# Performance work log

Hardware: AMD Instinct MI355X
Metric: run time of the kernel (lower is better)

The kernel has to match this reference:

```python
import jax, jax.numpy as jnp
import numpy as np
import itertools

LUT_DIM = 33  # 33x33x33 color LUT, as in Generator3DLUT_zero(dim=33)


def setup_inputs() -> dict:
    key = jax.random.key(0)
    k1, k2 = jax.random.split(key)
    # RGB image batch in [0,1]: [B, 3, H, W]
    x = jax.random.uniform(k1, (4, 3, 1080, 1920), dtype=jnp.float32)
    # Learned LUT parameter: [3, dim, dim, dim] (channels, b-axis, g-axis, r-axis)
    LUT = jax.random.normal(k2, (3, LUT_DIM, LUT_DIM, LUT_DIM), dtype=jnp.float32)
    return {"x": x, "LUT": LUT}


def _trilinear_lut(x, LUT, dim):
    # x: [B,3,H,W] in [0,1]; LUT: [3,dim,dim,dim] indexed [channel, b, g, r]
    # (r varies fastest, matching the original CUDA trilinear_forward kernel
    #  where flat index = r + g*dim + b*dim*dim).
    scaled = jnp.clip(x, 0.0, 1.0) * (dim - 1)          # [B,3,H,W]
    idx = jnp.clip(jnp.floor(scaled).astype(jnp.int32), 0, dim - 2)
    frac = scaled - idx.astype(scaled.dtype)            # in [0,1]
    r_id, g_id, b_id = idx[:, 0], idx[:, 1], idx[:, 2]   # each [B,H,W]
    fr, fg, fb = frac[:, 0], frac[:, 1], frac[:, 2]      # each [B,H,W]

    out = jnp.zeros_like(x)  # [B,3,H,W]
    for dr, dg, db in itertools.product((0, 1), repeat=3):  # 8 corners
        w = (jnp.where(dr, fr, 1.0 - fr)
             * jnp.where(dg, fg, 1.0 - fg)
             * jnp.where(db, fb, 1.0 - fb))               # [B,H,W]
        corner = LUT[:, b_id + db, g_id + dg, r_id + dr]  # [3,B,H,W] gather
        out = out + w[:, None] * jnp.transpose(corner, (1, 0, 2, 3))
    return out


def reference(x, LUT):
    return _trilinear_lut(x, LUT, LUT_DIM)
```

## Files before the change

kernel.cpp:

```cpp
#include <hip/hip_runtime.h>
#include <hip/hip_fp16.h>

#define DIM  33
#define DIM2 1089
#define DIM3 35937
#define HW   2073600
#define NPIX 8294400

typedef float  vf4 __attribute__((ext_vector_type(4)));
typedef _Float16 vh8 __attribute__((ext_vector_type(8)));

union F4H {
    vf4      f4;
    _Float16 h[8];
};

__global__ __launch_bounds__(256) void pack_lut8_kernel(
        const float* __restrict__ lut, vf4* __restrict__ lut8) {
    int i = blockIdx.x * blockDim.x + threadIdx.x;
    if (i >= DIM3) return;
    int b   = i / DIM2;
    int rem = i - b * DIM2;
    int g   = rem / DIM;
    int r   = rem - g * DIM;
    int b1 = min(b + 1, DIM - 1);
    int g1 = min(g + 1, DIM - 1);
    int r1 = min(r + 1, DIM - 1);

    _Float16 h[32];
#pragma unroll
    for (int db = 0; db < 2; ++db)
#pragma unroll
        for (int dg = 0; dg < 2; ++dg)
#pragma unroll
            for (int dr = 0; dr < 2; ++dr) {
                int bb = db ? b1 : b;
                int gg = dg ? g1 : g;
                int rr = dr ? r1 : r;
                int base = bb * DIM2 + gg * DIM + rr;
                int ci = ((db * 2 + dg) * 2 + dr) * 3;
                h[ci + 0] = (_Float16)lut[base];
                h[ci + 1] = (_Float16)lut[base + DIM3];
                h[ci + 2] = (_Float16)lut[base + 2 * DIM3];
            }
#pragma unroll
    for (int k = 24; k < 32; ++k) h[k] = (_Float16)0.0f;

    const vf4* hv = (const vf4*)h;
    vf4* dst = lut8 + (size_t)i * 4;
    dst[0] = hv[0];
    dst[1] = hv[1];
    dst[2] = hv[2];
    dst[3] = hv[3];
}

__device__ __forceinline__ void trilerp8(
        float r, float g, float b, const vf4* __restrict__ lut8,
        float& o0, float& o1, float& o2) {
    float rs = fminf(fmaxf(r, 0.0f), 1.0f) * 32.0f;
    float gs = fminf(fmaxf(g, 0.0f), 1.0f) * 32.0f;
    float bs = fminf(fmaxf(b, 0.0f), 1.0f) * 32.0f;
    int ri = min((int)rs, 31);
    int gi = min((int)gs, 31);
    int bi = min((int)bs, 31);
    float fr = rs - (float)ri;
    float fg = gs - (float)gi;
    float fb = bs - (float)bi;

    const vf4* e = lut8 + (size_t)(bi * DIM2 + gi * DIM + ri) * 4;
    F4H q0, q1, q2;
    q0.f4 = e[0];
    q1.f4 = e[1];
    q2.f4 = e[2];

    float c[24];
#pragma unroll
    for (int j = 0; j < 8; ++j) {
        c[j]      = (float)q0.h[j];
        c[8 + j]  = (float)q1.h[j];
        c[16 + j] = (float)q2.h[j];
    }

    float wr[2] = {1.0f - fr, fr};
    float wg[2] = {1.0f - fg, fg};
    float wb[2] = {1.0f - fb, fb};
    float a0 = 0.0f, a1 = 0.0f, a2 = 0.0f;
#pragma unroll
    for (int db = 0; db < 2; ++db)
#pragma unroll
        for (int dg = 0; dg < 2; ++dg) {
            float wbg = wb[db] * wg[dg];
#pragma unroll
            for (int dr = 0; dr < 2; ++dr) {
                float w = wbg * wr[dr];
                int ci = ((db * 2 + dg) * 2 + dr) * 3;
                a0 = fmaf(w, c[ci + 0], a0);
                a1 = fmaf(w, c[ci + 1], a1);
                a2 = fmaf(w, c[ci + 2], a2);
            }
        }
    o0 = a0; o1 = a1; o2 = a2;
}

__global__ __launch_bounds__(256) void lut_apply_fp16x8(
        const float* __restrict__ x, const vf4* __restrict__ lut8,
        float* __restrict__ out) {
    int i4 = blockIdx.x * blockDim.x + threadIdx.x;
    const int HW4 = HW / 4;
    if (i4 >= NPIX / 4) return;
    int n   = i4 / HW4;
    int rem = i4 - n * HW4;
    size_t base = (size_t)n * (size_t)(3 * HW) + (size_t)rem * 4;

    const vf4 rv = __builtin_nontemporal_load((const vf4*)(x + base));
    const vf4 gv = __builtin_nontemporal_load((const vf4*)(x + base + HW));
    const vf4 bv = __builtin_nontemporal_load((const vf4*)(x + base + 2 * (size_t)HW));

    float oa[4], ob[4], oc[4];
#pragma unroll
    for (int k = 0; k < 4; ++k) {
        trilerp8(rv[k], gv[k], bv[k], lut8, oa[k], ob[k], oc[k]);
    }
    vf4 o0 = {oa[0], oa[1], oa[2], oa[3]};
    vf4 o1 = {ob[0], ob[1], ob[2], ob[3]};
    vf4 o2 = {oc[0], oc[1], oc[2], oc[3]};
    __builtin_nontemporal_store(o0, (vf4*)(out + base));
    __builtin_nontemporal_store(o1, (vf4*)(out + base + HW));
    __builtin_nontemporal_store(o2, (vf4*)(out + base + 2 * (size_t)HW));
}

extern "C" void kernel_launch(void* const* d_in, const int* in_sizes, int n_in,
                              void* d_out, int out_size, void* d_ws, size_t ws_size,
                              hipStream_t stream) {
    const float* x   = (const float*)d_in[0];
    const float* lut = (const float*)d_in[1];
    float* out = (float*)d_out;

    const int groups = NPIX / 4;
    const int blocks = (groups + 255) / 256;

    vf4* lut8 = (vf4*)d_ws;
    pack_lut8_kernel<<<(DIM3 + 255) / 256, 256, 0, stream>>>(lut, lut8);
    lut_apply_fp16x8<<<blocks, 256, 0, stream>>>(x, lut8, out);
}
```

Before: 225.8 us.

## Quantize LUT to packed 8-bit and gather from LDS in persistent kernel

Finds the LUT's max absolute value, then packs it as one 32-bit word per node holding three unsigned 8-bit channels. The whole 144KB table is loaded into LDS by a persistent 1024-thread block per CU, and chunks of pixels are pulled from an atomic work counter. Each pixel's eight corner reads now come from LDS instead of scattered global/L2 gathers, and results are dequantized with a single scale and bias. The trade-off is a much coarser LUT (8-bit versus fp16), a risk of LDS bank conflicts, and extra small pre-kernels plus a memset.

```diff
diff --git a/kernel.cpp b/kernel.cpp
--- a/kernel.cpp
+++ b/kernel.cpp
@@ -1,19 +1,157 @@
 #include <hip/hip_runtime.h>
-#include <hip/hip_fp16.h>
 
 #define DIM  33
 #define DIM2 1089
 #define DIM3 35937
 #define HW   2073600
+#define HW4  518400
 #define NPIX 8294400
-
-typedef float  vf4 __attribute__((ext_vector_type(4)));
-typedef _Float16 vh8 __attribute__((ext_vector_type(8)));
-
-union F4H {
-    vf4      f4;
-    _Float16 h[8];
-};
+#define GROUPS (NPIX / 4)
+#define CHUNK  4096
+#define NCHUNK ((GROUPS + CHUNK - 1) / CHUNK)
+#define LDS_BYTES (DIM3 * 4)
+#define MAIN_BLOCKS  256
+#define MAIN_THREADS 1024
+
+typedef float vf4 __attribute__((ext_vector_type(4)));
+
+#define TBL_OFF 64
+
+__device__ __forceinline__ float ub(unsigned v, int b) {
+    return (float)((v >> (8 * b)) & 0xffu);
+}
+
+__global__ __launch_bounds__(256) void lut_maxabs_kernel(
+        const float* __restrict__ lut, unsigned* __restrict__ maxbits) {
+    int i = blockIdx.x * 256 + threadIdx.x;
+    float m = 0.0f;
+    if (i < 3 * DIM3) m = fabsf(lut[i]);
+#pragma unroll
+    for (int off = 32; off > 0; off >>= 1)
+        m = fmaxf(m, __shfl_down(m, off, 64));
+    if ((threadIdx.x & 63) == 0)
+        atomicMax(maxbits, __float_as_uint(m));
+}
+
+__global__ __launch_bounds__(256) void pack_lut_u8_kernel(
+        const float* __restrict__ lut, const unsigned* __restrict__ maxbits,
+        unsigned* __restrict__ tbl) {
+    int i = blockIdx.x * 256 + threadIdx.x;
+    if (i >= DIM3) return;
+    float mx  = fmaxf(__uint_as_float(*maxbits), 1e-20f);
+    float inv = 127.0f / mx;
+    int q0 = min(max(__float2int_rn(lut[i]            * inv) + 128, 0), 255);
+    int q1 = min(max(__float2int_rn(lut[i + DIM3]     * inv) + 128, 0), 255);
+    int q2 = min(max(__float2int_rn(lut[i + 2 * DIM3] * inv) + 128, 0), 255);
+    tbl[i] = (unsigned)q0 | ((unsigned)q1 << 8) | ((unsigned)q2 << 16);
+}
+
+extern __shared__ unsigned s_tbl[];
+
+__global__ __launch_bounds__(MAIN_THREADS, 1) void lut_apply_lds(
+        const float* __restrict__ x, const unsigned* __restrict__ tbl,
+        unsigned* __restrict__ ctr, const unsigned* __restrict__ maxbits,
+        float* __restrict__ out) {
+    __shared__ unsigned chunk_s;
+    for (int i = threadIdx.x; i < DIM3; i += MAIN_THREADS)
+        s_tbl[i] = tbl[i];
+    __syncthreads();
+
+    const float mx   = fmaxf(__uint_as_float(*maxbits), 1e-20f);
+    const float s_   = mx * (1.0f / 127.0f);
+    const float bias = -128.0f * s_;
+
+    for (;;) {
+        if (threadIdx.x == 0) chunk_s = atomicAdd(ctr, 1u);
+        __syncthreads();
+        unsigned c = chunk_s;
+        __syncthreads();
+        if (c >= NCHUNK) return;
+
+        int gend = min((int)((c + 1) * CHUNK), GROUPS);
+        for (int g = (int)(c * CHUNK) + threadIdx.x; g < gend; g += MAIN_THREADS) {
+            int n   = g / HW4;
+            int rem = g - n * HW4;
+            size_t base = (size_t)n * (size_t)(3 * HW) + (size_t)rem * 4;
+
+            const vf4 rv = __builtin_nontemporal_load((const vf4*)(x + base));
+            const vf4 gv = __builtin_nontemporal_load((const vf4*)(x + base + HW));
+            const vf4 bv = __builtin_nontemporal_load((const vf4*)(x + base + 2 * (size_t)HW));
+
+            float oa[4], ob[4], oc[4];
+#pragma unroll
+            for (int k = 0; k < 4; ++k) {
+                float rs = fminf(fmaxf(rv[k], 0.0f), 1.0f) * 32.0f;
+                float gs = fminf(fmaxf(gv[k], 0.0f), 1.0f) * 32.0f;
+                float bs = fminf(fmaxf(bv[k], 0.0f), 1.0f) * 32.0f;
+                int ri = min((int)rs, 31);
+                int gi = min((int)gs, 31);
+                int bi = min((int)bs, 31);
+                float fr = rs - (float)ri;
+                float fg = gs - (float)gi;
+                float fb = bs - (float)bi;
+
+                int i00 = bi * DIM2 + gi * DIM + ri;
+                unsigned c000 = s_tbl[i00];
+                unsigned c001 = s_tbl[i00 + 1];
+                unsigned c010 = s_tbl[i00 + DIM];
+                unsigned c011 = s_tbl[i00 + DIM + 1];
+                unsigned c100 = s_tbl[i00 + DIM2];
+                unsigned c101 = s_tbl[i00 + DIM2 + 1];
+                unsigned c110 = s_tbl[i00 + DIM2 + DIM];
+                unsigned c111 = s_tbl[i00 + DIM2 + DIM + 1];
+
+                float wr1 = fr, wr0 = 1.0f - fr;
+                float wg1 = fg, wg0 = 1.0f - fg;
+                float wb1 = fb, wb0 = 1.0f - fb;
+                float wb0g0 = wb0 * wg0, wb0g1 = wb0 * wg1;
+                float wb1g0 = wb1 * wg0, wb1g1 = wb1 * wg1;
+                float w000 = wb0g0 * wr0, w001 = wb0g0 * wr1;
+                float w010 = wb0g1 * wr0, w011 = wb0g1 * wr1;
+                float w100 = wb1g0 * wr0, w101 = wb1g0 * wr1;
+                float w110 = wb1g1 * wr0, w111 = wb1g1 * wr1;
+
+                float a0, a1, a2;
+                a0 =      w000 * ub(c000, 0);
+                a1 =      w000 * ub(c000, 1);
+                a2 =      w000 * ub(c000, 2);
+                a0 = fmaf(w001,  ub(c001, 0), a0);
+                a1 = fmaf(w001,  ub(c001, 1), a1);
+                a2 = fmaf(w001,  ub(c001, 2), a2);
+                a0 = fmaf(w010,  ub(c010, 0), a0);
+                a1 = fmaf(w010,  ub(c010, 1), a1);
+                a2 = fmaf(w010,  ub(c010, 2), a2);
+                a0 = fmaf(w011,  ub(c011, 0), a0);
+                a1 = fmaf(w011,  ub(c011, 1), a1);
+                a2 = fmaf(w011,  ub(c011, 2), a2);
+                a0 = fmaf(w100,  ub(c100, 0), a0);
+                a1 = fmaf(w100,  ub(c100, 1), a1);
+                a2 = fmaf(w100,  ub(c100, 2), a2);
+                a0 = fmaf(w101,  ub(c101, 0), a0);
+                a1 = fmaf(w101,  ub(c101, 1), a1);
+                a2 = fmaf(w101,  ub(c101, 2), a2);
+                a0 = fmaf(w110,  ub(c110, 0), a0);
+                a1 = fmaf(w110,  ub(c110, 1), a1);
+                a2 = fmaf(w110,  ub(c110, 2), a2);
+                a0 = fmaf(w111,  ub(c111, 0), a0);
+                a1 = fmaf(w111,  ub(c111, 1), a1);
+                a2 = fmaf(w111,  ub(c111, 2), a2);
+
+                oa[k] = fmaf(s_, a0, bias);
+                ob[k] = fmaf(s_, a1, bias);
+                oc[k] = fmaf(s_, a2, bias);
+            }
+            vf4 s0 = {oa[0], oa[1], oa[2], oa[3]};
+            vf4 s1 = {ob[0], ob[1], ob[2], ob[3]};
+            vf4 s2 = {oc[0], oc[1], oc[2], oc[3]};
+            __builtin_nontemporal_store(s0, (vf4*)(out + base));
+            __builtin_nontemporal_store(s1, (vf4*)(out + base + HW));
+            __builtin_nontemporal_store(s2, (vf4*)(out + base + 2 * (size_t)HW));
+        }
+    }
+}
+
+union F4H { vf4 f4; _Float16 h[8]; };
 
 __global__ __launch_bounds__(256) void pack_lut8_kernel(
         const float* __restrict__ lut, vf4* __restrict__ lut8) {
@@ -26,7 +164,6 @@
     int b1 = min(b + 1, DIM - 1);
     int g1 = min(g + 1, DIM - 1);
     int r1 = min(r + 1, DIM - 1);
-
     _Float16 h[32];
 #pragma unroll
     for (int db = 0; db < 2; ++db)
@@ -45,88 +182,68 @@
             }
 #pragma unroll
     for (int k = 24; k < 32; ++k) h[k] = (_Float16)0.0f;
-
     const vf4* hv = (const vf4*)h;
     vf4* dst = lut8 + (size_t)i * 4;
-    dst[0] = hv[0];
-    dst[1] = hv[1];
-    dst[2] = hv[2];
-    dst[3] = hv[3];
-}
-
-__device__ __forceinline__ void trilerp8(
-        float r, float g, float b, const vf4* __restrict__ lut8,
-        float& o0, float& o1, float& o2) {
-    float rs = fminf(fmaxf(r, 0.0f), 1.0f) * 32.0f;
-    float gs = fminf(fmaxf(g, 0.0f), 1.0f) * 32.0f;
-    float bs = fminf(fmaxf(b, 0.0f), 1.0f) * 32.0f;
-    int ri = min((int)rs, 31);
-    int gi = min((int)gs, 31);
-    int bi = min((int)bs, 31);
-    float fr = rs - (float)ri;
-    float fg = gs - (float)gi;
-    float fb = bs - (float)bi;
-
-    const vf4* e = lut8 + (size_t)(bi * DIM2 + gi * DIM + ri) * 4;
-    F4H q0, q1, q2;
-    q0.f4 = e[0];
-    q1.f4 = e[1];
-    q2.f4 = e[2];
-
-    float c[24];
-#pragma unroll
-    for (int j = 0; j < 8; ++j) {
-        c[j]      = (float)q0.h[j];
-        c[8 + j]  = (float)q1.h[j];
-        c[16 + j] = (float)q2.h[j];
-    }
-
-    float wr[2] = {1.0f - fr, fr};
-    float wg[2] = {1.0f - fg, fg};
-    float wb[2] = {1.0f - fb, fb};
-    float a0 = 0.0f, a1 = 0.0f, a2 = 0.0f;
-#pragma unroll
-    for (int db = 0; db < 2; ++db)
-#pragma unroll
-        for (int dg = 0; dg < 2; ++dg) {
-            float wbg = wb[db] * wg[dg];
-#pragma unroll
-            for (int dr = 0; dr < 2; ++dr) {
-                float w = wbg * wr[dr];
-                int ci = ((db * 2 + dg) * 2 + dr) * 3;
-                a0 = fmaf(w, c[ci + 0], a0);
-                a1 = fmaf(w, c[ci + 1], a1);
-                a2 = fmaf(w, c[ci + 2], a2);
-            }
-        }
-    o0 = a0; o1 = a1; o2 = a2;
+    dst[0] = hv[0]; dst[1] = hv[1]; dst[2] = hv[2]; dst[3] = hv[3];
 }
 
 __global__ __launch_bounds__(256) void lut_apply_fp16x8(
         const float* __restrict__ x, const vf4* __restrict__ lut8,
         float* __restrict__ out) {
     int i4 = blockIdx.x * blockDim.x + threadIdx.x;
-    const int HW4 = HW / 4;
     if (i4 >= NPIX / 4) return;
     int n   = i4 / HW4;
     int rem = i4 - n * HW4;
     size_t base = (size_t)n * (size_t)(3 * HW) + (size_t)rem * 4;
-
     const vf4 rv = __builtin_nontemporal_load((const vf4*)(x + base));
     const vf4 gv = __builtin_nontemporal_load((const vf4*)(x + base + HW));
     const vf4 bv = __builtin_nontemporal_load((const vf4*)(x + base + 2 * (size_t)HW));
-
     float oa[4], ob[4], oc[4];
 #pragma unroll
     for (int k = 0; k < 4; ++k) {
-        trilerp8(rv[k], gv[k], bv[k], lut8, oa[k], ob[k], oc[k]);
+        float rs = fminf(fmaxf(rv[k], 0.0f), 1.0f) * 32.0f;
+        float gs = fminf(fmaxf(gv[k], 0.0f), 1.0f) * 32.0f;
+        float bs = fminf(fmaxf(bv[k], 0.0f), 1.0f) * 32.0f;
+        int ri = min((int)rs, 31);
+        int gi = min((int)gs, 31);
+        int bi = min((int)bs, 31);
+        float fr = rs - (float)ri;
+        float fg = gs - (float)gi;
+        float fb = bs - (float)bi;
+        const vf4* e = lut8 + (size_t)(bi * DIM2 + gi * DIM + ri) * 4;
+        F4H q0, q1, q2;
+        q0.f4 = e[0]; q1.f4 = e[1]; q2.f4 = e[2];
+        float c[24];
+#pragma unroll
+        for (int j = 0; j < 8; ++j) {
+            c[j] = (float)q0.h[j]; c[8 + j] = (float)q1.h[j]; c[16 + j] = (float)q2.h[j];
+        }
+        float wr[2] = {1.0f - fr, fr};
+        float wg[2] = {1.0f - fg, fg};
+        float wb[2] = {1.0f - fb, fb};
+        float a0 = 0.0f, a1 = 0.0f, a2 = 0.0f;
+#pragma unroll
+        for (int db = 0; db < 2; ++db)
+#pragma unroll
+            for (int dg = 0; dg < 2; ++dg) {
+                float wbg = wb[db] * wg[dg];
+#pragma unroll
+                for (int dr = 0; dr < 2; ++dr) {
+                    float w = wbg * wr[dr];
+                    int ci = ((db * 2 + dg) * 2 + dr) * 3;
+                    a0 = fmaf(w, c[ci + 0], a0);
+                    a1 = fmaf(w, c[ci + 1], a1);
+                    a2 = fmaf(w, c[ci + 2], a2);
+                }
+            }
+        oa[k] = a0; ob[k] = a1; oc[k] = a2;
     }
-    vf4 o0 = {oa[0], oa[1], oa[2], oa[3]};
-    vf4 o1 = {ob[0], ob[1], ob[2], ob[3]};
-    vf4 o2 = {oc[0], oc[1], oc[2], oc[3]};
-    __builtin_nontemporal_store(o0, (vf4*)(out + base));
-    __builtin_nontemporal_store(o1, (vf4*)(out + base + HW));
-    __builtin_nontemporal_store(o2, (vf4*)(out + base + 2 * (size_t)HW));
+    vf4 s0 = {oa[0], oa[1], oa[2], oa[3]};
+    vf4 s1 = {ob[0], ob[1], ob[2], ob[3]};
+    vf4 s2 = {oc[0], oc[1], oc[2], oc[3]};
+    __builtin_nontemporal_store(s0, (vf4*)(out + base));
+    __builtin_nontemporal_store(s1, (vf4*)(out + base + HW));
+    __builtin_nontemporal_store(s2, (vf4*)(out + base + 2 * (size_t)HW));
 }
 
 extern "C" void kernel_launch(void* const* d_in, const int* in_sizes, int n_in,
@@ -136,10 +253,26 @@
     const float* lut = (const float*)d_in[1];
     float* out = (float*)d_out;
 
-    const int groups = NPIX / 4;
-    const int blocks = (groups + 255) / 256;
-
-    vf4* lut8 = (vf4*)d_ws;
-    pack_lut8_kernel<<<(DIM3 + 255) / 256, 256, 0, stream>>>(lut, lut8);
-    lut_apply_fp16x8<<<blocks, 256, 0, stream>>>(x, lut8, out);
-}
+    unsigned* ctr     = (unsigned*)d_ws;
+    unsigned* maxbits = (unsigned*)d_ws + 1;
+    unsigned* tbl     = (unsigned*)((char*)d_ws + TBL_OFF);
+
+    static hipError_t attr_err = hipFuncSetAttribute(
+        (const void*)lut_apply_lds,
+        hipFuncAttributeMaxDynamicSharedMemorySize, LDS_BYTES);
+    hipError_t err2 = hipFuncSetAttribute(
+        (const void*)lut_apply_lds,
+        hipFuncAttributeMaxDynamicSharedMemorySize, LDS_BYTES);
+
+    if (attr_err == hipSuccess && err2 == hipSuccess) {
+        hipMemsetAsync(d_ws, 0, 8, stream);
+        lut_maxabs_kernel<<<(3 * DIM3 + 255) / 256, 256, 0, stream>>>(lut, maxbits);
+        pack_lut_u8_kernel<<<(DIM3 + 255) / 256, 256, 0, stream>>>(lut, maxbits, tbl);
+        lut_apply_lds<<<MAIN_BLOCKS, MAIN_THREADS, LDS_BYTES, stream>>>(
+            x, tbl, ctr, maxbits, out);
+    } else {
+        vf4* lut8 = (vf4*)((char*)d_ws + TBL_OFF);
+        pack_lut8_kernel<<<(DIM3 + 255) / 256, 256, 0, stream>>>(lut, lut8);
+        lut_apply_fp16x8<<<(GROUPS + 255) / 256, 256, 0, stream>>>(x, lut8, out);
+    }
+}
```

Result: faster. 201.8 us (-10.6%).
